# Kernel tuning notes

Measured on AMD Instinct MI355X. Metric: run time of the kernel, lower is better.

The kernel has to match this reference:

```python
import jax, jax.numpy as jnp
import numpy as np

N = 100000      # patches per bag
L, H, D = 1024, 512, 256   # size_dict['small']
K = 64          # k_sample
NC = 2          # n_classes


def setup_inputs() -> dict:
    key = jax.random.key(0)
    ks = jax.random.split(key, 12)
    s = 0.02
    return {
        "h": jax.random.normal(ks[0], (N, L), dtype=jnp.float32),
        "W1": jax.random.normal(ks[1], (L, H), dtype=jnp.float32) * s,
        "b1": jnp.zeros((H,), jnp.float32),
        "Wa": jax.random.normal(ks[2], (H, D), dtype=jnp.float32) * s,
        "ba": jnp.zeros((D,), jnp.float32),
        "Wb": jax.random.normal(ks[3], (H, D), dtype=jnp.float32) * s,
        "bb": jnp.zeros((D,), jnp.float32),
        "Wc": jax.random.normal(ks[4], (D, 1), dtype=jnp.float32) * s,
        "bc": jnp.zeros((1,), jnp.float32),
        "Winst": jax.random.normal(ks[5], (H, 2), dtype=jnp.float32) * s,
        "binst": jnp.zeros((2,), jnp.float32),
        "Wcls": jax.random.normal(ks[6], (H, NC), dtype=jnp.float32) * s,
        "bcls": jnp.zeros((NC,), jnp.float32),
        "label": 1,
    }


def reference(h, W1, b1, Wa, ba, Wb, bb, Wc, bc, Winst, binst, Wcls, bcls, label):
    # fc: Linear(1024,512) + ReLU
    h1 = jax.nn.relu(h @ W1 + b1)                      # [N, 512]
    # gated attention net
    a = jnp.tanh(h1 @ Wa + ba)                         # [N, 256]
    g = jax.nn.sigmoid(h1 @ Wb + bb)                   # [N, 256]
    A = (a * g) @ Wc + bc                              # [N, 1]
    A = A.T                                            # [1, N]
    A_raw = A
    A = jax.nn.softmax(A, axis=1)                      # [1, N]

    # instance evaluation: top-k / bottom-k select + gather + tiny classifier
    Asq = A[0]                                         # [N]
    _, top_p_ids = jax.lax.top_k(Asq, K)
    _, top_n_ids = jax.lax.top_k(-Asq, K)
    all_inst = jnp.concatenate([h1[top_p_ids], h1[top_n_ids]], axis=0)  # [2K, 512]
    inst_logits = all_inst @ Winst + binst             # [2K, 2]
    all_preds = jnp.argmax(inst_logits, axis=1)
    p_targets = jnp.full((K,), label, dtype=jnp.int32)
    n_targets = jnp.zeros((K,), dtype=jnp.int32)
    all_targets = jnp.concatenate([p_targets, n_targets], axis=0)
    logp = jax.nn.log_softmax(inst_logits, axis=1)
    instance_loss = -jnp.mean(logp[jnp.arange(2 * K), all_targets])

    # bag-level aggregation and classifier
    M = A @ h1                                         # [1, 512]
    logits = M @ Wcls + bcls                           # [1, n_classes]
    Y_hat = jnp.argmax(logits, axis=1, keepdims=True)
    Y_prob = jax.nn.softmax(logits, axis=1)
    return logits, Y_prob, Y_hat, A_raw, instance_loss, all_preds, all_targets
```

## Files before the change

### kernel.cpp

```cpp
#include <hip/hip_runtime.h>

#define NN 100000
#define LL 1024
#define HH 512
#define DD 256
#define TOPK 64
#define CAP 3072
#define CPB 4
#define DELTA 3e-3f

#define WS_W1T   0u
#define WS_B2    1048576u
#define WS_Z     1572864u
#define Z_MNUM   0u
#define Z_SEXP   2048u
#define Z_LOSS   2052u
#define Z_CNTT   2056u
#define Z_CNTB   2060u
#define Z_HIST   2064u
#define Z_WSA    10256u
#define Z_PARAMS 410384u
#define Z_SEL    410416u
#define Z_CANDT  410928u
#define Z_CANDB  423216u
#define Z_AEXT   435504u
#define Z_AEXB   447792u
#define Z_ZWORDS 108876

typedef float  f32x16 __attribute__((ext_vector_type(16)));
typedef short  bf16x8 __attribute__((ext_vector_type(8)));

#define MFMA(a,b,c) __builtin_amdgcn_mfma_f32_32x32x16_bf16(a,b,c,0,0,0)

__device__ __forceinline__ unsigned short f2bf(float x){
  unsigned u = __float_as_uint(x);
  u += 0x7FFFu + ((u >> 16) & 1u);
  return (unsigned short)(u >> 16);
}
__device__ __forceinline__ float bf2f(unsigned short v){
  return __uint_as_float(((unsigned)v) << 16);
}
__device__ __forceinline__ unsigned sortable_u(float f){
  unsigned u = __float_as_uint(f);
  return (u & 0x80000000u) ? ~u : (u | 0x80000000u);
}
__device__ __forceinline__ float inv_sortable(unsigned u){
  unsigned orig = (u & 0x80000000u) ? (u ^ 0x80000000u) : ~u;
  return __uint_as_float(orig);
}
__device__ __forceinline__ unsigned cvtpk(float lo, float hi){
  unsigned r;
  asm("v_cvt_pk_bf16_f32 %0, %1, %2" : "=v"(r) : "v"(lo), "v"(hi));
  return r;
}

__global__ void k0_prep(const float* __restrict__ W1, const float* __restrict__ Wa,
                        const float* __restrict__ Wb,
                        unsigned short* __restrict__ W1T, unsigned short* __restrict__ B2,
                        unsigned* __restrict__ zwords)
{
  const int n1 = HH * LL;
  const int n2 = HH * HH;
  const int tot = n1 + n2 + Z_ZWORDS;
  int stride = gridDim.x * 256;
  for (int idx = blockIdx.x * 256 + threadIdx.x; idx < tot; idx += stride){
    if (idx < n1){
      int k = idx >> 9, n = idx & 511;
      W1T[(size_t)n * LL + k] = f2bf(W1[idx]);
    } else if (idx < n1 + n2){
      int j = idx - n1;
      int k = j >> 9, n = j & 511;
      int w = n >> 6, ii = n & 63;
      float v = (ii < 32) ? Wa[k * DD + (w * 32 + ii)] : Wb[k * DD + (w * 32 + ii - 32)];
      B2[(size_t)n * HH + k] = f2bf(v);
    } else {
      zwords[idx - n1 - n2] = 0u;
    }
  }
}

__global__ __launch_bounds__(512, 2)
void k_mega(const float* __restrict__ h, const unsigned short* __restrict__ W1T,
            const unsigned short* __restrict__ B2g,
            const float* __restrict__ b1, const float* __restrict__ ba,
            const float* __restrict__ bbg, const float* __restrict__ Wc,
            const float* __restrict__ bc,
            float* __restrict__ outA,
            float* __restrict__ wsA,
            float* __restrict__ Mnum, float* __restrict__ sum_exp)
{
  __shared__ __align__(16) unsigned short SM[64 * 512];

  const int tid  = threadIdx.x;
  const int wid  = tid >> 6;
  const int lane = tid & 63;
  const int l31  = lane & 31;
  const int half = lane >> 5;
  const int r0   = blockIdx.x * 64;

  const int sr = tid >> 3;
  const int sc = (tid & 7) << 2;
  int gr = r0 + sr; if (gr > NN - 1) gr = NN - 1;
  const float* hp = h + (size_t)gr * LL + sc;

  const unsigned short* bp0 = W1T + (size_t)(wid * 64 + l31) * LL + half * 8;
  const unsigned short* bp1 = W1T + (size_t)(wid * 64 + 32 + l31) * LL + half * 8;

  f32x16 acc00 = (f32x16)0.f, acc01 = (f32x16)0.f, acc10 = (f32x16)0.f, acc11 = (f32x16)0.f;

  unsigned short* sbuf0 = SM;
  unsigned short* sbuf1 = SM + 2560;

  float4 av;
  {
    float4 a0 = *(const float4*)(hp);
    av = *(const float4*)(hp + 32);
    uint2 pk; pk.x = cvtpk(a0.x, a0.y); pk.y = cvtpk(a0.z, a0.w);
    *(uint2*)(sbuf0 + sr * 40 + sc) = pk;
  }
  asm volatile("s_waitcnt lgkmcnt(0)" ::: "memory");
  __builtin_amdgcn_s_barrier();
  __builtin_amdgcn_sched_barrier(0);

  unsigned short* rb = sbuf0;
  unsigned short* wb = sbuf1;

  #pragma unroll 1
  for (int kc = 0; kc < 32; ++kc){
    bf16x8 b00 = *(const bf16x8*)(bp0 + kc * 32);
    bf16x8 b10 = *(const bf16x8*)(bp1 + kc * 32);
    bf16x8 b01 = *(const bf16x8*)(bp0 + kc * 32 + 16);
    bf16x8 b11 = *(const bf16x8*)(bp1 + kc * 32 + 16);
    __builtin_amdgcn_sched_barrier(0);
    float4 cur = av;
    av = *(const float4*)(hp + min(kc + 2, 31) * 32);
    __builtin_amdgcn_sched_barrier(0);
    uint2 pk; pk.x = cvtpk(cur.x, cur.y); pk.y = cvtpk(cur.z, cur.w);
    *(uint2*)(wb + sr * 40 + sc) = pk;
    const unsigned short* a0p = rb + l31 * 40 + half * 8;
    const unsigned short* a1p = rb + (32 + l31) * 40 + half * 8;
    bf16x8 a0k0 = *(const bf16x8*)(a0p);
    bf16x8 a1k0 = *(const bf16x8*)(a1p);
    acc00 = MFMA(a0k0, b00, acc00); acc01 = MFMA(a0k0, b10, acc01);
    acc10 = MFMA(a1k0, b00, acc10); acc11 = MFMA(a1k0, b10, acc11);
    bf16x8 a0k1 = *(const bf16x8*)(a0p + 16);
    bf16x8 a1k1 = *(const bf16x8*)(a1p + 16);
    acc00 = MFMA(a0k1, b01, acc00); acc01 = MFMA(a0k1, b11, acc01);
    acc10 = MFMA(a1k1, b01, acc10); acc11 = MFMA(a1k1, b11, acc11);
    { unsigned short* t = rb; rb = wb; wb = t; }
    asm volatile("s_waitcnt lgkmcnt(0)" ::: "memory");
    __builtin_amdgcn_sched_barrier(0);
    __builtin_amdgcn_s_barrier();
    __builtin_amdgcn_sched_barrier(0);
  }
  __syncthreads();

  {
    float b1v0 = b1[wid * 64 + l31];
    float b1v1 = b1[wid * 64 + 32 + l31];
    int cb0 = wid * 8 + (l31 >> 3);
    int cb1 = wid * 8 + 4 + (l31 >> 3);
    int wi = l31 & 7;
    #pragma unroll
    for (int reg = 0; reg < 16; ++reg){
      int rA = (reg & 3) + ((reg >> 2) << 3) + (half << 2);
      int rB = rA + 32;
      float v;
      v = fmaxf(acc00[reg] + b1v0, 0.f); SM[rA * 512 + ((cb0 ^ (rA & 7)) << 3) + wi] = f2bf(v);
      v = fmaxf(acc01[reg] + b1v1, 0.f); SM[rA * 512 + ((cb1 ^ (rA & 7)) << 3) + wi] = f2bf(v);
      v = fmaxf(acc10[reg] + b1v0, 0.f); SM[rB * 512 + ((cb0 ^ (rB & 7)) << 3) + wi] = f2bf(v);
      v = fmaxf(acc11[reg] + b1v1, 0.f); SM[rB * 512 + ((cb1 ^ (rB & 7)) << 3) + wi] = f2bf(v);
    }
  }
  __syncthreads();

  f32x16 q00 = (f32x16)0.f, q01 = (f32x16)0.f, q10 = (f32x16)0.f, q11 = (f32x16)0.f;
  const unsigned short* c0p = B2g + (size_t)(wid * 64 + l31) * HH + half * 8;
  const unsigned short* c1p = B2g + (size_t)(wid * 64 + 32 + l31) * HH + half * 8;
  const int m0x = l31 & 7;
  #pragma unroll 1
  for (int kc = 0; kc < 16; ++kc){
    #pragma unroll
    for (int ks = 0; ks < 2; ++ks){
      int ko = kc * 32 + ks * 16;
      int sw = (((kc * 4 + ks * 2 + half) ^ m0x) << 3);
      bf16x8 a0 = *(const bf16x8*)(SM + l31 * 512 + sw);
      bf16x8 a1 = *(const bf16x8*)(SM + (32 + l31) * 512 + sw);
      bf16x8 b0 = *(const bf16x8*)(c0p + ko);
      bf16x8 b1 = *(const bf16x8*)(c1p + ko);
      q00 = MFMA(a0, b0, q00); q01 = MFMA(a0, b1, q01);
      q10 = MFMA(a1, b0, q10); q11 = MFMA(a1, b1, q11);
    }
  }

  {
    int ca = wid * 32 + l31;
    float bav = ba[ca], bbv = bbg[ca], wcv = Wc[ca];
    #pragma unroll
    for (int mt = 0; mt < 2; ++mt){
      #pragma unroll
      for (int reg = 0; reg < 16; ++reg){
        float pav = (mt ? q10[reg] : q00[reg]) + bav;
        float pbv = (mt ? q11[reg] : q01[reg]) + bbv;
        float p = tanhf(pav) * (1.f / (1.f + expf(-pbv))) * wcv;
        p += __shfl_xor(p, 1, 64);  p += __shfl_xor(p, 2, 64);
        p += __shfl_xor(p, 4, 64);  p += __shfl_xor(p, 8, 64);
        p += __shfl_xor(p, 16, 64);
        if (l31 == 0){
          int rl = mt * 32 + (reg & 3) + ((reg >> 2) << 3) + (half << 2);
          atomicAdd(&wsA[r0 + rl], p);
        }
      }
    }
  }
  __syncthreads();
  if (tid < 64){
    int g = r0 + tid;
    if (g < NN){
      float Ar = atomicAdd(&wsA[g], 0.0f) + bc[0];
      outA[g] = Ar;
    }
  }
  __syncthreads();

  float ev = 0.f;
  { int g = r0 + lane; if (g < NN) ev = expf(outA[g]); }
  float pm = 0.f;
  const int tch = tid >> 3, twi = tid & 7;
  #pragma unroll 4
  for (int r = 0; r < 64; ++r){
    float e = __shfl(ev, r, 64);
    pm += e * bf2f(SM[r * 512 + ((tch ^ (r & 7)) << 3) + twi]);
  }
  atomicAdd(&Mnum[tid], pm);
  if (wid == 0){
    float s = ev;
    s += __shfl_xor(s, 1, 64);  s += __shfl_xor(s, 2, 64);  s += __shfl_xor(s, 4, 64);
    s += __shfl_xor(s, 8, 64);  s += __shfl_xor(s, 16, 64); s += __shfl_xor(s, 32, 64);
    if (lane == 0) atomicAdd(sum_exp, s);
  }
}

__global__ void k_hist(const float* __restrict__ A, unsigned* __restrict__ hist)
{
  __shared__ unsigned lh[2048];
  for (int i = threadIdx.x; i < 2048; i += 256) lh[i] = 0u;
  __syncthreads();
  for (int i = blockIdx.x * 256 + threadIdx.x; i < NN; i += gridDim.x * 256)
    atomicAdd(&lh[sortable_u(A[i]) >> 21], 1u);
  __syncthreads();
  for (int i = threadIdx.x; i < 2048; i += 256)
    if (lh[i]) atomicAdd(&hist[i], lh[i]);
}

__global__ void k_scan(const unsigned* __restrict__ hist, unsigned* __restrict__ params)
{
  if (threadIdx.x == 0){
    unsigned c = 0, hh = 0; int b = 2047;
    for (; b >= 0; --b){ hh = hist[b]; c += hh; if (c >= TOPK) break; }
    if (b < 0) b = 0;
    params[2] = (unsigned)b;
    params[4] = TOPK - (c - hh);
    c = 0; hh = 0; int b2 = 0;
    for (; b2 < 2048; ++b2){ hh = hist[b2]; c += hh; if (c >= TOPK) break; }
    if (b2 > 2047) b2 = 2047;
    params[3] = (unsigned)b2;
    params[5] = TOPK - (c - hh);
  }
}

__global__ void k_hist2(const float* __restrict__ A, const unsigned* __restrict__ params,
                        unsigned* __restrict__ h2T, unsigned* __restrict__ h2B)
{
  __shared__ unsigned lh[4096];
  for (int i = threadIdx.x; i < 4096; i += 256) lh[i] = 0u;
  __syncthreads();
  unsigned bT = params[2], bB = params[3];
  for (int i = blockIdx.x * 256 + threadIdx.x; i < NN; i += gridDim.x * 256){
    unsigned u = sortable_u(A[i]);
    unsigned b = u >> 21;
    if (b == bT) atomicAdd(&lh[(u >> 10) & 2047u], 1u);
    if (b == bB) atomicAdd(&lh[2048 + ((u >> 10) & 2047u)], 1u);
  }
  __syncthreads();
  for (int i = threadIdx.x; i < 2048; i += 256){
    if (lh[i])        atomicAdd(&h2T[i], lh[i]);
    if (lh[2048 + i]) atomicAdd(&h2B[i], lh[2048 + i]);
  }
}

__global__ __launch_bounds__(128)
void k_scan2(const unsigned* __restrict__ h2T, const unsigned* __restrict__ h2B,
             unsigned* __restrict__ params)
{
  int side = threadIdx.x >> 6;
  int lane = threadIdx.x & 63;
  const unsigned* h2 = side ? h2B : h2T;
  unsigned bT  = params[2 + side];
  unsigned rem = params[4 + side];
  unsigned cs = 0;
  int base = lane * 32;
  #pragma unroll 4
  for (int j = 0; j < 32; ++j) cs += h2[base + j];
  unsigned before = 0;
  for (int j = 0; j < 64; ++j){
    unsigned v = __shfl(cs, j, 64);
    bool earlier = side ? (j < lane) : (j > lane);
    if (earlier) before += v;
  }
  if (before < rem && before + cs >= rem){
    unsigned c = before; int s = base;
    if (side == 0){
      for (int b = base + 31; b >= base; --b){ c += h2[b]; if (c >= rem){ s = b; break; } }
      unsigned ulo = (bT << 21) | ((unsigned)s << 10);
      float v = inv_sortable(ulo) - DELTA;
      params[0] = sortable_u(v);
    } else {
      for (int b = base; b < base + 32; ++b){ c += h2[b]; if (c >= rem){ s = b; break; } }
      unsigned uhi = (bT << 21) | ((unsigned)s << 10) | 1023u;
      float v = inv_sortable(uhi) + DELTA;
      params[1] = sortable_u(v);
    }
  }
}

__global__ void k_collect(const float* __restrict__ A, const unsigned* __restrict__ params,
                          unsigned* cntT, unsigned* cntB,
                          unsigned* __restrict__ candT, unsigned* __restrict__ candB)
{
  unsigned p0 = params[0], p1 = params[1];
  for (int i = blockIdx.x * 256 + threadIdx.x; i < NN; i += gridDim.x * 256){
    unsigned u = sortable_u(A[i]);
    if (u >= p0){ unsigned pos = atomicAdd(cntT, 1u); if (pos < CAP) candT[pos] = (unsigned)i; }
    if (u <= p1){ unsigned pos = atomicAdd(cntB, 1u); if (pos < CAP) candB[pos] = (unsigned)i; }
  }
}

__global__ __launch_bounds__(256)
void k_exact(const float* __restrict__ h, const float* __restrict__ W1, const float* __restrict__ b1,
             const float* __restrict__ Wa, const float* __restrict__ ba,
             const float* __restrict__ Wb, const float* __restrict__ bbg,
             const float* __restrict__ Wc, const float* __restrict__ bc,
             const unsigned* cntT, const unsigned* cntB,
             const unsigned* __restrict__ candT, const unsigned* __restrict__ candB,
             float* __restrict__ AexT, float* __restrict__ AexB)
{
  const int PB = CAP / CPB;
  int b = blockIdx.x;
  int side = (b >= PB) ? 1 : 0;
  int base = (side ? b - PB : b) * CPB;
  unsigned cnt = side ? *cntB : *cntT;
  if (cnt > CAP) cnt = CAP;
  if (base >= (int)cnt) return;
  int nc = min(CPB, (int)cnt - base);
  const unsigned* cand = side ? candB : candT;
  float* Aex = side ? AexB : AexT;

  __shared__ float hrow[CPB][LL];
  __shared__ float h1row[CPB][HH];
  __shared__ unsigned rows_s[CPB];
  __shared__ float red[4][CPB];
  int tid = threadIdx.x;
  if (tid < CPB) rows_s[tid] = cand[base + min(tid, nc - 1)];
  __syncthreads();
  for (int c = 0; c < CPB; ++c)
    ((float4*)hrow[c])[tid] = ((const float4*)(h + (size_t)rows_s[c] * LL))[tid];
  __syncthreads();

  float s0[CPB], s1[CPB];
  { float v0 = b1[tid], v1 = b1[tid + 256];
    #pragma unroll
    for (int c = 0; c < CPB; ++c){ s0[c] = v0; s1[c] = v1; } }
  for (int k = 0; k < LL; ++k){
    float w0 = W1[k * HH + tid];
    float w1 = W1[k * HH + tid + 256];
    #pragma unroll
    for (int c = 0; c < CPB; ++c){ float hv = hrow[c][k]; s0[c] += hv * w0; s1[c] += hv * w1; }
  }
  #pragma unroll
  for (int c = 0; c < CPB; ++c){
    h1row[c][tid] = fmaxf(s0[c], 0.f);
    h1row[c][tid + 256] = fmaxf(s1[c], 0.f);
  }
  __syncthreads();

  float pa[CPB], pb[CPB];
  float bav = ba[tid], bbv = bbg[tid], wcv = Wc[tid];
  #pragma unroll
  for (int c = 0; c < CPB; ++c){ pa[c] = bav; pb[c] = bbv; }
  for (int k = 0; k < HH; ++k){
    float wav = Wa[k * DD + tid];
    float wbv = Wb[k * DD + tid];
    #pragma unroll
    for (int c = 0; c < CPB; ++c){ float hv = h1row[c][k]; pa[c] += hv * wav; pb[c] += hv * wbv; }
  }
  int lane = tid & 63, w = tid >> 6;
  #pragma unroll
  for (int c = 0; c < CPB; ++c){
    float p = tanhf(pa[c]) * (1.f / (1.f + expf(-pb[c]))) * wcv;
    p += __shfl_xor(p, 1, 64);  p += __shfl_xor(p, 2, 64);  p += __shfl_xor(p, 4, 64);
    p += __shfl_xor(p, 8, 64);  p += __shfl_xor(p, 16, 64); p += __shfl_xor(p, 32, 64);
    if (lane == 0) red[w][c] = p;
  }
  __syncthreads();
  if (tid == 0)
    for (int c = 0; c < nc; ++c)
      Aex[base + c] = red[0][c] + red[1][c] + red[2][c] + red[3][c] + bc[0];
}

__global__ __launch_bounds__(256)
void k_select(const unsigned* cntT, const unsigned* cntB,
              const unsigned* __restrict__ candT, const unsigned* __restrict__ candB,
              const float* __restrict__ AexT, const float* __restrict__ AexB,
              unsigned* __restrict__ sel)
{
  __shared__ unsigned long long keys[CAP];
  __shared__ unsigned long long wmax[4];
  __shared__ unsigned long long best_s;
  int tid = threadIdx.x;
  for (int side = 0; side < 2; ++side){
    unsigned cnt = side ? *cntB : *cntT; if (cnt > CAP) cnt = CAP;
    const unsigned* cand = side ? candB : candT;
    const float* Aex = side ? AexB : AexT;
    for (int j = tid; j < (int)cnt; j += 256){
      unsigned su = sortable_u(Aex[j]);
      if (side) su = ~su;
      keys[j] = (((unsigned long long)su) << 32) | (unsigned long long)(0xFFFFFFFFu - cand[j]);
    }
    __syncthreads();
    for (int it = 0; it < TOPK; ++it){
      unsigned long long loc = 0ull;
      for (int j = tid; j < (int)cnt; j += 256){ unsigned long long k = keys[j]; loc = (k > loc) ? k : loc; }
      for (int off = 1; off < 64; off <<= 1){
        unsigned long long o = __shfl_xor(loc, off, 64);
        loc = (o > loc) ? o : loc;
      }
      if ((tid & 63) == 0) wmax[tid >> 6] = loc;
      __syncthreads();
      if (tid == 0){
        unsigned long long m01 = (wmax[0] > wmax[1]) ? wmax[0] : wmax[1];
        unsigned long long m23 = (wmax[2] > wmax[3]) ? wmax[2] : wmax[3];
        unsigned long long bb_ = (m01 > m23) ? m01 : m23;
        best_s = bb_;
        sel[side * TOPK + it] = 0xFFFFFFFFu - (unsigned)(bb_ & 0xFFFFFFFFull);
      }
      __syncthreads();
      unsigned long long bv = best_s;
      for (int j = tid; j < (int)cnt; j += 256) if (keys[j] == bv) keys[j] = 0ull;
      __syncthreads();
    }
    __syncthreads();
  }
}

__global__ __launch_bounds__(256)
void k_inst(const float* __restrict__ h, const float* __restrict__ W1, const float* __restrict__ b1,
            const float* __restrict__ Winst, const float* __restrict__ binst,
            const unsigned* __restrict__ sel, const int* __restrict__ labelp,
            float* __restrict__ out, float* __restrict__ loss_sum)
{
  __shared__ float hrow[LL];
  __shared__ float h1row[HH];
  __shared__ float red[4][2];
  int i = blockIdx.x, tid = threadIdx.x;
  unsigned row = sel[i];
  ((float4*)hrow)[tid] = ((const float4*)(h + (size_t)row * LL))[tid];
  __syncthreads();
  float s0 = b1[tid], s1 = b1[tid + 256];
  for (int k = 0; k < LL; ++k){
    float hv = hrow[k];
    s0 += hv * W1[k * HH + tid];
    s1 += hv * W1[k * HH + tid + 256];
  }
  h1row[tid] = fmaxf(s0, 0.f); h1row[tid + 256] = fmaxf(s1, 0.f);
  __syncthreads();
  float l0 = 0.f, l1 = 0.f;
  for (int d = tid; d < HH; d += 256){
    float hv = h1row[d];
    l0 += hv * Winst[d * 2];
    l1 += hv * Winst[d * 2 + 1];
  }
  for (int off = 1; off < 64; off <<= 1){ l0 += __shfl_xor(l0, off, 64); l1 += __shfl_xor(l1, off, 64); }
  if ((tid & 63) == 0){ red[tid >> 6][0] = l0; red[tid >> 6][1] = l1; }
  __syncthreads();
  if (tid == 0){
    float L0 = red[0][0] + red[1][0] + red[2][0] + red[3][0] + binst[0];
    float L1 = red[0][1] + red[1][1] + red[2][1] + red[3][1] + binst[1];
    int lab = labelp[0];
    int tgt = (i < TOPK) ? lab : 0;
    out[100006 + i] = (L1 > L0) ? 1.f : 0.f;
    out[100134 + i] = (float)tgt;
    float m = fmaxf(L0, L1);
    float lse = m + logf(expf(L0 - m) + expf(L1 - m));
    float lp = ((tgt == 1) ? L1 : L0) - lse;
    atomicAdd(loss_sum, -lp);
  }
}

__global__ __launch_bounds__(512)
void k_final(const float* __restrict__ Mnum, const float* __restrict__ sum_exp,
             const float* __restrict__ Wcls, const float* __restrict__ bcls,
             const float* __restrict__ loss_sum, float* __restrict__ out)
{
  __shared__ float red[8][2];
  int tid = threadIdx.x;
  float S = *sum_exp;
  float m = Mnum[tid] / S;
  float p0 = m * Wcls[tid * 2], p1 = m * Wcls[tid * 2 + 1];
  for (int off = 1; off < 64; off <<= 1){ p0 += __shfl_xor(p0, off, 64); p1 += __shfl_xor(p1, off, 64); }
  if ((tid & 63) == 0){ red[tid >> 6][0] = p0; red[tid >> 6][1] = p1; }
  __syncthreads();
  if (tid == 0){
    float L0 = bcls[0], L1 = bcls[1];
    for (int w = 0; w < 8; ++w){ L0 += red[w][0]; L1 += red[w][1]; }
    out[0] = L0; out[1] = L1;
    float mm = fmaxf(L0, L1);
    float e0 = expf(L0 - mm), e1 = expf(L1 - mm);
    out[2] = e0 / (e0 + e1); out[3] = e1 / (e0 + e1);
    out[4] = (L1 > L0) ? 1.f : 0.f;
    out[100005] = loss_sum[0] / 128.f;
  }
}

extern "C" void kernel_launch(void* const* d_in, const int* in_sizes, int n_in,
                              void* d_out, int out_size, void* d_ws, size_t ws_size,
                              hipStream_t stream)
{
  const float* h     = (const float*)d_in[0];
  const float* W1    = (const float*)d_in[1];
  const float* b1    = (const float*)d_in[2];
  const float* Wa    = (const float*)d_in[3];
  const float* ba    = (const float*)d_in[4];
  const float* Wb    = (const float*)d_in[5];
  const float* bbg   = (const float*)d_in[6];
  const float* Wc    = (const float*)d_in[7];
  const float* bc    = (const float*)d_in[8];
  const float* Winst = (const float*)d_in[9];
  const float* binst = (const float*)d_in[10];
  const float* Wcls  = (const float*)d_in[11];
  const float* bcls  = (const float*)d_in[12];
  const int*   label = (const int*)d_in[13];
  float* out = (float*)d_out;

  char* ws = (char*)d_ws;
  unsigned short* W1T = (unsigned short*)(ws + WS_W1T);
  unsigned short* B2  = (unsigned short*)(ws + WS_B2);
  char* Z = ws + WS_Z;
  float*    Mnum   = (float*)(Z + Z_MNUM);
  float*    sexp   = (float*)(Z + Z_SEXP);
  float*    lsum   = (float*)(Z + Z_LOSS);
  unsigned* cntT   = (unsigned*)(Z + Z_CNTT);
  unsigned* cntB   = (unsigned*)(Z + Z_CNTB);
  unsigned* hist   = (unsigned*)(Z + Z_HIST);
  float*    wsA    = (float*)(Z + Z_WSA);
  unsigned* params = (unsigned*)(Z + Z_PARAMS);
  unsigned* sel    = (unsigned*)(Z + Z_SEL);
  unsigned* candT  = (unsigned*)(Z + Z_CANDT);
  unsigned* candB  = (unsigned*)(Z + Z_CANDB);
  float*    AexT   = (float*)(Z + Z_AEXT);
  float*    AexB   = (float*)(Z + Z_AEXB);
  unsigned* h2T    = (unsigned*)(Z + Z_CANDT);
  unsigned* h2B    = (unsigned*)(Z + Z_CANDB);

  k0_prep<<<1024, 256, 0, stream>>>(W1, Wa, Wb, W1T, B2, (unsigned*)Z);
  k_mega<<<1563, 512, 0, stream>>>(h, W1T, B2, b1, ba, bbg, Wc, bc,
                                   out + 5, wsA, Mnum, sexp);
  k_hist<<<400, 256, 0, stream>>>(out + 5, hist);
  k_scan<<<1, 64, 0, stream>>>(hist, params);
  k_hist2<<<400, 256, 0, stream>>>(out + 5, params, h2T, h2B);
  k_scan2<<<1, 128, 0, stream>>>(h2T, h2B, params);
  k_collect<<<400, 256, 0, stream>>>(out + 5, params, cntT, cntB, candT, candB);
  k_exact<<<2 * (CAP / CPB), 256, 0, stream>>>(h, W1, b1, Wa, ba, Wb, bbg, Wc, bc,
                                               cntT, cntB, candT, candB, AexT, AexB);
  k_select<<<1, 256, 0, stream>>>(cntT, cntB, candT, candB, AexT, AexB, sel);
  k_inst<<<128, 256, 0, stream>>>(h, W1, b1, Winst, binst, sel, label, out, lsum);
  k_final<<<1, 512, 0, stream>>>(Mnum, sexp, Wcls, bcls, lsum, out);
}
```

Before: 1.165 ms.

## Pre-swizzle weights into MFMA fragment layout and stage h in 256-wide K chunks

The prep kernel now converts W1, Wa and Wb into a fragment-major bf16 layout, so each lane's MFMA B operand becomes one contiguous 16-byte load with the wave's loads fully coalesced. It uses an LDS transpose to do this and needs only 128 blocks. The main GEMM now stages h in 256-column chunks in a swizzled LDS buffer and interleaves its loads with the MFMA sub-iterations. This replaces 32 barriers on small 32-column tiles with 4 barriers on larger chunks, cutting synchronisation and strided weight loads. The cost is larger LDS double buffers, which could limit occupancy, and more register pressure from the unrolled chunk loop.

```diff
diff --git a/kernel.cpp b/kernel.cpp
--- a/kernel.cpp
+++ b/kernel.cpp
@@ -54,34 +54,66 @@
   return r;
 }
 
-__global__ void k0_prep(const float* __restrict__ W1, const float* __restrict__ Wa,
-                        const float* __restrict__ Wb,
-                        unsigned short* __restrict__ W1T, unsigned short* __restrict__ B2,
-                        unsigned* __restrict__ zwords)
-{
-  const int n1 = HH * LL;
-  const int n2 = HH * HH;
-  const int tot = n1 + n2 + Z_ZWORDS;
-  int stride = gridDim.x * 256;
-  for (int idx = blockIdx.x * 256 + threadIdx.x; idx < tot; idx += stride){
-    if (idx < n1){
-      int k = idx >> 9, n = idx & 511;
-      W1T[(size_t)n * LL + k] = f2bf(W1[idx]);
-    } else if (idx < n1 + n2){
-      int j = idx - n1;
-      int k = j >> 9, n = j & 511;
-      int w = n >> 6, ii = n & 63;
-      float v = (ii < 32) ? Wa[k * DD + (w * 32 + ii)] : Wb[k * DD + (w * 32 + ii - 32)];
-      B2[(size_t)n * HH + k] = f2bf(v);
-    } else {
-      zwords[idx - n1 - n2] = 0u;
-    }
+__global__ __launch_bounds__(256)
+void k0_prep(const float* __restrict__ W1, const float* __restrict__ Wa,
+             const float* __restrict__ Wb,
+             unsigned short* __restrict__ W1F, unsigned short* __restrict__ B2F,
+             unsigned* __restrict__ zwords)
+{
+  __shared__ unsigned short T[16 * 512];
+  int b = blockIdx.x, tid = threadIdx.x;
+  if (b < 64){
+    int s = b;
+    #pragma unroll
+    for (int i = 0; i < 8; ++i){
+      int g = tid + 256 * i;
+      int kk = g >> 7, c4 = g & 127;
+      float4 v = *(const float4*)(W1 + (size_t)(16 * s + kk) * HH + c4 * 4);
+      uint2 pk; pk.x = cvtpk(v.x, v.y); pk.y = cvtpk(v.z, v.w);
+      *(uint2*)(T + kk * 512 + c4 * 4) = pk;
+    }
+    __syncthreads();
+    int c = tid >> 4, lbase = (tid & 15) * 4;
+    #pragma unroll
+    for (int q = 0; q < 4; ++q){
+      int l = lbase + q; int l31 = l & 31; int kh = l >> 5;
+      unsigned short tmp[8];
+      #pragma unroll
+      for (int j = 0; j < 8; ++j) tmp[j] = T[(kh * 8 + j) * 512 + c * 32 + l31];
+      *(bf16x8*)(W1F + ((size_t)(c * 64 + s) * 64 + l) * 8) = *(bf16x8*)tmp;
+    }
+  } else if (b < 96){
+    int s = b - 64;
+    #pragma unroll
+    for (int i = 0; i < 4; ++i){
+      int g = tid + 256 * i;
+      int kk = g >> 6, c4 = g & 63;
+      float4 va = *(const float4*)(Wa + (size_t)(16 * s + kk) * DD + c4 * 4);
+      float4 vb = *(const float4*)(Wb + (size_t)(16 * s + kk) * DD + c4 * 4);
+      uint2 pa; pa.x = cvtpk(va.x, va.y); pa.y = cvtpk(va.z, va.w);
+      uint2 pb; pb.x = cvtpk(vb.x, vb.y); pb.y = cvtpk(vb.z, vb.w);
+      *(uint2*)(T + kk * 512 + c4 * 4) = pa;
+      *(uint2*)(T + kk * 512 + 256 + c4 * 4) = pb;
+    }
+    __syncthreads();
+    int c = tid >> 4, lbase = (tid & 15) * 4;
+    int col0 = (c & 1) * 256 + (c >> 1) * 32;
+    #pragma unroll
+    for (int q = 0; q < 4; ++q){
+      int l = lbase + q; int l31 = l & 31; int kh = l >> 5;
+      unsigned short tmp[8];
+      #pragma unroll
+      for (int j = 0; j < 8; ++j) tmp[j] = T[(kh * 8 + j) * 512 + col0 + l31];
+      *(bf16x8*)(B2F + ((size_t)(c * 32 + s) * 64 + l) * 8) = *(bf16x8*)tmp;
+    }
+  } else {
+    for (int i = (b - 96) * 256 + tid; i < Z_ZWORDS; i += 32 * 256) zwords[i] = 0u;
   }
 }
 
 __global__ __launch_bounds__(512, 2)
-void k_mega(const float* __restrict__ h, const unsigned short* __restrict__ W1T,
-            const unsigned short* __restrict__ B2g,
+void k_mega(const float* __restrict__ h, const unsigned short* __restrict__ W1F,
+            const unsigned short* __restrict__ B2F,
             const float* __restrict__ b1, const float* __restrict__ ba,
             const float* __restrict__ bbg, const float* __restrict__ Wc,
             const float* __restrict__ bc,
@@ -98,62 +130,73 @@
   const int half = lane >> 5;
   const int r0   = blockIdx.x * 64;
 
-  const int sr = tid >> 3;
-  const int sc = (tid & 7) << 2;
-  int gr = r0 + sr; if (gr > NN - 1) gr = NN - 1;
-  const float* hp = h + (size_t)gr * LL + sc;
-
-  const unsigned short* bp0 = W1T + (size_t)(wid * 64 + l31) * LL + half * 8;
-  const unsigned short* bp1 = W1T + (size_t)(wid * 64 + 32 + l31) * LL + half * 8;
+  const int scol = tid & 63;
+  const int srow = tid >> 6;
+
+  const unsigned short* bp = W1F + (size_t)(2 * wid) * 32768 + (size_t)lane * 8;
 
   f32x16 acc00 = (f32x16)0.f, acc01 = (f32x16)0.f, acc10 = (f32x16)0.f, acc11 = (f32x16)0.f;
 
-  unsigned short* sbuf0 = SM;
-  unsigned short* sbuf1 = SM + 2560;
-
-  float4 av;
-  {
-    float4 a0 = *(const float4*)(hp);
-    av = *(const float4*)(hp + 32);
-    uint2 pk; pk.x = cvtpk(a0.x, a0.y); pk.y = cvtpk(a0.z, a0.w);
-    *(uint2*)(sbuf0 + sr * 40 + sc) = pk;
-  }
-  asm volatile("s_waitcnt lgkmcnt(0)" ::: "memory");
-  __builtin_amdgcn_s_barrier();
-  __builtin_amdgcn_sched_barrier(0);
-
-  unsigned short* rb = sbuf0;
-  unsigned short* wb = sbuf1;
+  unsigned short* buf0 = SM;
+  unsigned short* buf1 = SM + 64 * 256;
+
+  #pragma unroll
+  for (int j = 0; j < 8; ++j){
+    int r = srow + 8 * j;
+    int gr = r0 + r; if (gr > NN - 1) gr = NN - 1;
+    float4 v = *(const float4*)(h + (size_t)gr * LL + scol * 4);
+    uint2 pk; pk.x = cvtpk(v.x, v.y); pk.y = cvtpk(v.z, v.w);
+    *(uint2*)(buf0 + r * 256 + ((((scol >> 1) ^ (r & 31)) << 3) + (scol & 1) * 4)) = pk;
+  }
+  __syncthreads();
+
+  unsigned short* rb = buf0;
+  unsigned short* wb = buf1;
+
+#define SUBIT(i) { \
+    const int s0_ = sb + 2 * (i), s1_ = s0_ + 1; \
+    bf16x8 b00 = *(const bf16x8*)(bp + s0_ * 512); \
+    bf16x8 b01 = *(const bf16x8*)(bp + s1_ * 512); \
+    bf16x8 b10 = *(const bf16x8*)(bp + 32768 + s0_ * 512); \
+    bf16x8 b11 = *(const bf16x8*)(bp + 32768 + s1_ * 512); \
+    const int ck0 = 4 * (i) + half, ck1 = ck0 + 2; \
+    bf16x8 a0k0 = *(const bf16x8*)(rb + l31 * 256 + ((ck0 ^ l31) << 3)); \
+    bf16x8 a1k0 = *(const bf16x8*)(rb + (32 + l31) * 256 + ((ck0 ^ l31) << 3)); \
+    bf16x8 a0k1 = *(const bf16x8*)(rb + l31 * 256 + ((ck1 ^ l31) << 3)); \
+    bf16x8 a1k1 = *(const bf16x8*)(rb + (32 + l31) * 256 + ((ck1 ^ l31) << 3)); \
+    acc00 = MFMA(a0k0, b00, acc00); acc01 = MFMA(a0k0, b10, acc01); \
+    acc10 = MFMA(a1k0, b00, acc10); acc11 = MFMA(a1k0, b10, acc11); \
+    acc00 = MFMA(a0k1, b01, acc00); acc01 = MFMA(a0k1, b11, acc01); \
+    acc10 = MFMA(a1k1, b01, acc10); acc11 = MFMA(a1k1, b11, acc11); }
+
+#define LDH(dst, j) { \
+    int r_ = srow + 8 * (j); \
+    int gr_ = r0 + r_; if (gr_ > NN - 1) gr_ = NN - 1; \
+    dst = *(const float4*)(h + (size_t)gr_ * LL + coff + scol * 4); }
+
+#define WRH(v, j) { \
+    int r_ = srow + 8 * (j); \
+    uint2 pk_; pk_.x = cvtpk((v).x, (v).y); pk_.y = cvtpk((v).z, (v).w); \
+    *(uint2*)(wb + r_ * 256 + ((((scol >> 1) ^ (r_ & 31)) << 3) + (scol & 1) * 4)) = pk_; }
 
   #pragma unroll 1
-  for (int kc = 0; kc < 32; ++kc){
-    bf16x8 b00 = *(const bf16x8*)(bp0 + kc * 32);
-    bf16x8 b10 = *(const bf16x8*)(bp1 + kc * 32);
-    bf16x8 b01 = *(const bf16x8*)(bp0 + kc * 32 + 16);
-    bf16x8 b11 = *(const bf16x8*)(bp1 + kc * 32 + 16);
-    __builtin_amdgcn_sched_barrier(0);
-    float4 cur = av;
-    av = *(const float4*)(hp + min(kc + 2, 31) * 32);
-    __builtin_amdgcn_sched_barrier(0);
-    uint2 pk; pk.x = cvtpk(cur.x, cur.y); pk.y = cvtpk(cur.z, cur.w);
-    *(uint2*)(wb + sr * 40 + sc) = pk;
-    const unsigned short* a0p = rb + l31 * 40 + half * 8;
-    const unsigned short* a1p = rb + (32 + l31) * 40 + half * 8;
-    bf16x8 a0k0 = *(const bf16x8*)(a0p);
-    bf16x8 a1k0 = *(const bf16x8*)(a1p);
-    acc00 = MFMA(a0k0, b00, acc00); acc01 = MFMA(a0k0, b10, acc01);
-    acc10 = MFMA(a1k0, b00, acc10); acc11 = MFMA(a1k0, b10, acc11);
-    bf16x8 a0k1 = *(const bf16x8*)(a0p + 16);
-    bf16x8 a1k1 = *(const bf16x8*)(a1p + 16);
-    acc00 = MFMA(a0k1, b01, acc00); acc01 = MFMA(a0k1, b11, acc01);
-    acc10 = MFMA(a1k1, b01, acc10); acc11 = MFMA(a1k1, b11, acc11);
+  for (int ch = 0; ch < 4; ++ch){
+    const int sb = ch * 16;
+    const int coff = (ch + 1) * 256;
+    const bool st = (ch < 3);
+    float4 hA, hB;
+    if (st){ LDH(hA, 0) LDH(hB, 1) }
+    SUBIT(0) SUBIT(1)
+    if (st){ WRH(hA, 0) WRH(hB, 1) LDH(hA, 2) LDH(hB, 3) }
+    SUBIT(2) SUBIT(3)
+    if (st){ WRH(hA, 2) WRH(hB, 3) LDH(hA, 4) LDH(hB, 5) }
+    SUBIT(4) SUBIT(5)
+    if (st){ WRH(hA, 4) WRH(hB, 5) LDH(hA, 6) LDH(hB, 7) }
+    SUBIT(6) SUBIT(7)
+    if (st){ WRH(hA, 6) WRH(hB, 7) }
+    __syncthreads();
     { unsigned short* t = rb; rb = wb; wb = t; }
-    asm volatile("s_waitcnt lgkmcnt(0)" ::: "memory");
-    __builtin_amdgcn_sched_barrier(0);
-    __builtin_amdgcn_s_barrier();
-    __builtin_amdgcn_sched_barrier(0);
-  }
-  __syncthreads();
+  }
 
   {
     float b1v0 = b1[wid * 64 + l31];
@@ -175,19 +218,18 @@
   __syncthreads();
 
   f32x16 q00 = (f32x16)0.f, q01 = (f32x16)0.f, q10 = (f32x16)0.f, q11 = (f32x16)0.f;
-  const unsigned short* c0p = B2g + (size_t)(wid * 64 + l31) * HH + half * 8;
-  const unsigned short* c1p = B2g + (size_t)(wid * 64 + 32 + l31) * HH + half * 8;
+  const unsigned short* p2 = B2F + (size_t)(2 * wid) * 16384 + (size_t)lane * 8;
   const int m0x = l31 & 7;
   #pragma unroll 1
   for (int kc = 0; kc < 16; ++kc){
     #pragma unroll
     for (int ks = 0; ks < 2; ++ks){
-      int ko = kc * 32 + ks * 16;
+      int s = kc * 2 + ks;
+      bf16x8 b0 = *(const bf16x8*)(p2 + s * 512);
+      bf16x8 b1 = *(const bf16x8*)(p2 + 16384 + s * 512);
       int sw = (((kc * 4 + ks * 2 + half) ^ m0x) << 3);
       bf16x8 a0 = *(const bf16x8*)(SM + l31 * 512 + sw);
       bf16x8 a1 = *(const bf16x8*)(SM + (32 + l31) * 512 + sw);
-      bf16x8 b0 = *(const bf16x8*)(c0p + ko);
-      bf16x8 b1 = *(const bf16x8*)(c1p + ko);
       q00 = MFMA(a0, b0, q00); q01 = MFMA(a0, b1, q01);
       q10 = MFMA(a1, b0, q10); q11 = MFMA(a1, b1, q11);
     }
@@ -543,8 +585,8 @@
   float* out = (float*)d_out;
 
   char* ws = (char*)d_ws;
-  unsigned short* W1T = (unsigned short*)(ws + WS_W1T);
-  unsigned short* B2  = (unsigned short*)(ws + WS_B2);
+  unsigned short* W1F = (unsigned short*)(ws + WS_W1T);
+  unsigned short* B2F = (unsigned short*)(ws + WS_B2);
   char* Z = ws + WS_Z;
   float*    Mnum   = (float*)(Z + Z_MNUM);
   float*    sexp   = (float*)(Z + Z_SEXP);
@@ -562,8 +604,8 @@
   unsigned* h2T    = (unsigned*)(Z + Z_CANDT);
   unsigned* h2B    = (unsigned*)(Z + Z_CANDB);
 
-  k0_prep<<<1024, 256, 0, stream>>>(W1, Wa, Wb, W1T, B2, (unsigned*)Z);
-  k_mega<<<1563, 512, 0, stream>>>(h, W1T, B2, b1, ba, bbg, Wc, bc,
+  k0_prep<<<128, 256, 0, stream>>>(W1, Wa, Wb, W1F, B2F, (unsigned*)Z);
+  k_mega<<<1563, 512, 0, stream>>>(h, W1F, B2F, b1, ba, bbg, Wc, bc,
                                    out + 5, wsA, Mnum, sexp);
   k_hist<<<400, 256, 0, stream>>>(out + 5, hist);
   k_scan<<<1, 64, 0, stream>>>(hist, params);
```

Result: faster. 1.101 ms (-5.5%).
